# Optimization experiments

Measured on AMD Instinct MI355X. Metric: run time of the kernel, lower is better.

Reference implementation:

```python
import jax, jax.numpy as jnp
import numpy as np

EMBED_DIM = 1024
BATCH, SEQ = 4, 2048


def setup_inputs() -> dict:
    key = jax.random.key(0)
    k1, k2 = jax.random.split(key)
    hidden_states = jax.random.normal(k1, (BATCH, SEQ, EMBED_DIM), dtype=jnp.float32)
    # fused QKV projection weight (Linear(embed_dim, 3*embed_dim, bias=False)),
    # stored as [E, 3E] so y = x @ W
    W_qkv = jax.random.normal(k2, (EMBED_DIM, 3 * EMBED_DIM), dtype=jnp.float32) * (1.0 / np.sqrt(EMBED_DIM))
    return {"hidden_states": hidden_states, "W_qkv": W_qkv}


def reference(hidden_states, W_qkv):
    E = hidden_states.shape[-1]
    scale = 1.0 / np.sqrt(E)
    qkv = jnp.einsum('bse,ef->bsf', hidden_states, W_qkv)  # [B,S,3E]
    q, k, v = jnp.split(qkv, 3, axis=-1)                   # each [B,S,E]
    # scores = q @ (k^T * scale); softmax over keys
    scores = jnp.einsum('bqe,bke->bqk', q, k) * scale      # [B,S,S]
    w = jax.nn.softmax(scores, axis=-1)
    return jnp.einsum('bqk,bke->bqe', w, v)                # [B,S,E]
```

## Files before the change

kernel.cpp:

```cpp
#include <hip/hip_runtime.h>

typedef __attribute__((ext_vector_type(8))) short short8;
typedef __attribute__((ext_vector_type(8))) unsigned short ushort8;
typedef __attribute__((ext_vector_type(4))) float f32x4;

__device__ __forceinline__ float bf2f(unsigned short u) {
  union { unsigned int u; float f; } c; c.u = ((unsigned int)u) << 16; return c.f;
}
__device__ __forceinline__ unsigned short f2bf(float f) {
  union { float f; unsigned int u; } c; c.f = f;
  unsigned int x = c.u;
  return (unsigned short)((x + 0x7FFFu + ((x >> 16) & 1u)) >> 16);
}

#define GLD_LDS16(g, l)                                                        \
  __builtin_amdgcn_global_load_lds(                                            \
      (const __attribute__((address_space(1))) void*)(g),                      \
      (__attribute__((address_space(3))) void*)(l), 16, 0, 0)

__device__ __forceinline__ void bar() {
  asm volatile("" ::: "memory");
  __builtin_amdgcn_s_barrier();
  asm volatile("" ::: "memory");
}

__global__ __launch_bounds__(256) void prep_kernel(
    const float* __restrict__ X, unsigned short* __restrict__ Xb,
    const float* __restrict__ W, unsigned short* __restrict__ Wt,
    float* __restrict__ Lrow) {
  const int t = threadIdx.x;
  if (blockIdx.x < 4096) {
    long i = ((long)blockIdx.x * 256 + t) * 8;
    float4 a = *(const float4*)(X + i);
    float4 b = *(const float4*)(X + i + 4);
    ushort8 o;
    o[0] = f2bf(a.x); o[1] = f2bf(a.y); o[2] = f2bf(a.z); o[3] = f2bf(a.w);
    o[4] = f2bf(b.x); o[5] = f2bf(b.y); o[6] = f2bf(b.z); o[7] = f2bf(b.w);
    *(ushort8*)(Xb + i) = o;
  } else if (blockIdx.x < 4864) {
    const int bid = blockIdx.x - 4096;
    const int f0 = (bid % 48) * 64;
    const int e0 = (bid / 48) * 64;
    __shared__ unsigned short tile[64][65];
    const int cg = (t & 15) * 4;
    const int r = t >> 4;
#pragma unroll
    for (int i = 0; i < 4; ++i) {
      int e = r + i * 16;
      float4 v = *(const float4*)(W + (long)(e0 + e) * 3072 + f0 + cg);
      tile[e][cg + 0] = f2bf(v.x);
      tile[e][cg + 1] = f2bf(v.y);
      tile[e][cg + 2] = f2bf(v.z);
      tile[e][cg + 3] = f2bf(v.w);
    }
    __syncthreads();
#pragma unroll
    for (int i = 0; i < 4; ++i) {
      int f = (t >> 4) + i * 16;
      int e = (t & 15) * 4;
      ushort4 o;
      o.x = tile[e + 0][f];
      o.y = tile[e + 1][f];
      o.z = tile[e + 2][f];
      o.w = tile[e + 3][f];
      *(ushort4*)(Wt + (long)(f0 + f) * 1024 + e0 + e) = o;
    }
  } else {
    float4 z = {0.f, 0.f, 0.f, 0.f};
#pragma unroll
    for (int j = 0; j < 8; ++j) *(float4*)(Lrow + (j * 256 + t) * 4) = z;
  }
}

template <int MODE>
__device__ __forceinline__ void gemm256_body(
    const unsigned short* __restrict__ A, const unsigned short* __restrict__ B,
    void* __restrict__ Cv, int K, int lda, int ldb, int ldc,
    long sA, long sB, long sC, float alpha, float* __restrict__ Lrow,
    unsigned short* __restrict__ Vt) {
  __shared__ __align__(16) unsigned short smem[65536];

  const int t = threadIdx.x;
  const int lane = t & 63;
  const int wave = t >> 6;
  const int quad = lane >> 4;
  const int mrow = lane & 15;
  const int wm = wave >> 2;
  const int wn = wave & 3;

  const int bx = blockIdx.x, by = blockIdx.y, b = blockIdx.z;
  const int rowA0 = by * 256;
  const int rowB0 = bx * 256;
  const unsigned short* Ab = A + (long)b * sA;
  const unsigned short* Bb = B + (long)b * sB;

  const int srow = lane >> 2;
  const int schunk = (lane & 3) * 8;

  f32x4 acc[8][4];
#pragma unroll
  for (int i = 0; i < 8; ++i)
#pragma unroll
    for (int j = 0; j < 4; ++j) {
      f32x4 z = {0.f, 0.f, 0.f, 0.f};
      acc[i][j] = z;
    }

  const int NT = K >> 6;

  auto stg = [&](const unsigned short* gb, int ld, int r0, int kt, int kh,
                 int roff) {
#pragma unroll
    for (int j = 0; j < 2; ++j)
      GLD_LDS16(gb + (long)(r0 + j * 128 + wave * 16 + srow) * ld + kt +
                    kh * 32 + schunk,
                smem + roff + (j * 128 + wave * 16) * 32);
  };

  stg(Ab, lda, rowA0, 0, 0, 0);
  stg(Bb, ldb, rowB0, 0, 0, 16384);
  stg(Ab, lda, rowA0, 0, 1, 8192);
  stg(Bb, ldb, rowB0, 0, 1, 24576);
  stg(Bb, ldb, rowB0, 64, 0, 32768 + 16384);
  stg(Ab, lda, rowA0, 64, 0, 32768);
  asm volatile("s_waitcnt vmcnt(4)" ::: "memory");
  bar();

  const int rA_base = wm * 128 + mrow;
  const int rB_base = wn * 64 + mrow;
  const int qoff = quad * 8;

  for (int T = 0; T < NT; ++T) {
    const int buf = (T & 1) << 15;
    const int nbuf = buf ^ 32768;
    const unsigned short* A0 = smem + buf;
    const unsigned short* A1 = smem + buf + 8192;
    const unsigned short* B0 = smem + buf + 16384;
    const unsigned short* B1 = smem + buf + 24576;
    const int ktn = (T + 1) << 6;
    const int ktn2 = (T + 2) << 6;
    short8 af[4], bf[4];

#pragma unroll
    for (int i = 0; i < 4; ++i)
      af[i] = *(const short8*)(A0 + (rA_base + i * 16) * 32 + qoff);
#pragma unroll
    for (int j = 0; j < 4; ++j)
      bf[j] = *(const short8*)(B0 + (rB_base + j * 16) * 32 + qoff);
    if (T + 1 < NT) stg(Ab, lda, rowA0, ktn, 1, nbuf + 8192);
    bar();
    __builtin_amdgcn_sched_barrier(0);
    __builtin_amdgcn_s_setprio(1);
#pragma unroll
    for (int i = 0; i < 4; ++i)
#pragma unroll
      for (int j = 0; j < 4; ++j)
        acc[i][j] = __builtin_amdgcn_mfma_f32_16x16x32_bf16(af[i], bf[j],
                                                            acc[i][j], 0, 0, 0);
    __builtin_amdgcn_s_setprio(0);
    __builtin_amdgcn_sched_barrier(0);
    bar();

#pragma unroll
    for (int i = 0; i < 4; ++i)
      af[i] = *(const short8*)(A0 + (rA_base + 64 + i * 16) * 32 + qoff);
    if (T + 1 < NT) stg(Bb, ldb, rowB0, ktn, 1, nbuf + 24576);
    bar();
    __builtin_amdgcn_sched_barrier(0);
    __builtin_amdgcn_s_setprio(1);
#pragma unroll
    for (int i = 0; i < 4; ++i)
#pragma unroll
      for (int j = 0; j < 4; ++j)
        acc[4 + i][j] = __builtin_amdgcn_mfma_f32_16x16x32_bf16(
            af[i], bf[j], acc[4 + i][j], 0, 0, 0);
    __builtin_amdgcn_s_setprio(0);
    __builtin_amdgcn_sched_barrier(0);
    bar();

#pragma unroll
    for (int i = 0; i < 4; ++i)
      af[i] = *(const short8*)(A1 + (rA_base + i * 16) * 32 + qoff);
#pragma unroll
    for (int j = 0; j < 4; ++j)
      bf[j] = *(const short8*)(B1 + (rB_base + j * 16) * 32 + qoff);
    if (T + 2 < NT) stg(Bb, ldb, rowB0, ktn2, 0, buf + 16384);
    bar();
    __builtin_amdgcn_sched_barrier(0);
    __builtin_amdgcn_s_setprio(1);
#pragma unroll
    for (int i = 0; i < 4; ++i)
#pragma unroll
      for (int j = 0; j < 4; ++j)
        acc[i][j] = __builtin_amdgcn_mfma_f32_16x16x32_bf16(af[i], bf[j],
                                                            acc[i][j], 0, 0, 0);
    __builtin_amdgcn_s_setprio(0);
    __builtin_amdgcn_sched_barrier(0);
    bar();

#pragma unroll
    for (int i = 0; i < 4; ++i)
      af[i] = *(const short8*)(A1 + (rA_base + 64 + i * 16) * 32 + qoff);
    if (T + 2 < NT) stg(Ab, lda, rowA0, ktn2, 0, buf);
    bar();
    __builtin_amdgcn_sched_barrier(0);
    __builtin_amdgcn_s_setprio(1);
#pragma unroll
    for (int i = 0; i < 4; ++i)
#pragma unroll
      for (int j = 0; j < 4; ++j)
        acc[4 + i][j] = __builtin_amdgcn_mfma_f32_16x16x32_bf16(
            af[i], bf[j], acc[4 + i][j], 0, 0, 0);
    __builtin_amdgcn_s_setprio(0);
    __builtin_amdgcn_sched_barrier(0);
    if (T + 2 < NT) {
      asm volatile("s_waitcnt vmcnt(4)" ::: "memory");
    } else if (T + 1 < NT) {
      asm volatile("s_waitcnt vmcnt(0)" ::: "memory");
    }
    bar();
  }

  const long cb = (long)b * sC;

  if constexpr (MODE == 0) {
    if (bx < 8) {
      unsigned short* C = (unsigned short*)Cv;
#pragma unroll
      for (int m = 0; m < 8; ++m) {
        int row = rowA0 + wm * 128 + m * 16 + quad * 4;
#pragma unroll
        for (int j = 0; j < 4; ++j) {
          int col = rowB0 + wn * 64 + j * 16 + mrow;
#pragma unroll
          for (int r = 0; r < 4; ++r)
            C[(long)(row + r) * ldc + col] = f2bf(acc[m][j][r]);
        }
      }
    } else {
#pragma unroll
      for (int m = 0; m < 8; ++m) {
        int s4 = wm * 128 + m * 16 + quad * 4;
#pragma unroll
        for (int j = 0; j < 4; ++j) {
          int e = wn * 64 + j * 16 + mrow;
          int swz = ((e & 7) << 4) ^ (((e >> 3) & 3) << 3);
          ushort4 pk;
          pk.x = f2bf(acc[m][j][0]);
          pk.y = f2bf(acc[m][j][1]);
          pk.z = f2bf(acc[m][j][2]);
          pk.w = f2bf(acc[m][j][3]);
          *(ushort4*)(smem + e * 256 + (s4 ^ swz)) = pk;
        }
      }
      __syncthreads();
      const int batch = by >> 3;
      const int s_base = (by & 7) * 256;
      const int e_base = (bx - 8) * 256;
      unsigned short* VtB = Vt + (long)batch * 1024 * 2048;
      const int er = t >> 5;
      const int s = (t & 31) * 8;
#pragma unroll
      for (int rnd = 0; rnd < 16; ++rnd) {
        int e = rnd * 16 + er;
        int swz = ((e & 7) << 4) ^ (((e >> 3) & 3) << 3);
        ushort8 v = *(const ushort8*)(smem + e * 256 + (s ^ swz));
        *(ushort8*)(VtB + (long)(e_base + e) * 2048 + s_base + s) = v;
      }
    }
  } else {
    unsigned short* C = (unsigned short*)Cv;
    float p[8][4];
#pragma unroll
    for (int m = 0; m < 8; ++m)
#pragma unroll
      for (int r = 0; r < 4; ++r) p[m][r] = 0.f;
#pragma unroll
    for (int m = 0; m < 8; ++m) {
      int row = rowA0 + wm * 128 + m * 16 + quad * 4;
#pragma unroll
      for (int j = 0; j < 4; ++j) {
        int col = rowB0 + wn * 64 + j * 16 + mrow;
#pragma unroll
        for (int r = 0; r < 4; ++r) {
          float e = __expf(acc[m][j][r] * alpha);
          C[cb + (long)(row + r) * ldc + col] = f2bf(e);
          p[m][r] += e;
        }
      }
    }
#pragma unroll
    for (int off = 1; off < 16; off <<= 1)
#pragma unroll
      for (int m = 0; m < 8; ++m)
#pragma unroll
        for (int r = 0; r < 4; ++r)
          p[m][r] += __shfl_xor(p[m][r], off, 64);
    if (mrow == 0) {
#pragma unroll
      for (int m = 0; m < 8; ++m) {
        int row = rowA0 + wm * 128 + m * 16 + quad * 4;
#pragma unroll
        for (int r = 0; r < 4; ++r)
          atomicAdd(&Lrow[b * 2048 + row + r], p[m][r]);
      }
    }
  }
}

template <int MODE>
__device__ __forceinline__ void gemm_body(
    const unsigned short* __restrict__ A, const unsigned short* __restrict__ B,
    void* __restrict__ Cv, int K, int lda, int ldb, int ldc,
    long sA, long sB, long sC, float alpha, float* __restrict__ Lrow,
    unsigned short* __restrict__ Vt) {
  constexpr int BM = 128, BN = 128, BK = 64;
  __shared__ __align__(16) unsigned short smem[BM * BK + BN * BK];
  unsigned short* As = smem;
  unsigned short* Bs = smem + BM * BK;

  const int t = threadIdx.x;
  const int lane = t & 63;
  const int wave = t >> 6;
  const int quad = lane >> 4;
  const int mrow = lane & 15;
  const int wm = wave >> 1, wn = wave & 1;

  const int bx = blockIdx.x, by = blockIdx.y;
  const int rowA0 = by * BM;
  const int rowB0 = bx * BN;
  const int b = blockIdx.z;
  const unsigned short* Ab = A + (long)b * sA;
  const unsigned short* Bb = B + (long)b * sB;

  f32x4 acc[4][4];
#pragma unroll
  for (int i = 0; i < 4; ++i)
#pragma unroll
    for (int j = 0; j < 4; ++j) {
      f32x4 z = {0.f, 0.f, 0.f, 0.f};
      acc[i][j] = z;
    }

  const int rbase = wave * 32 + (lane >> 3);
  const int c2 = lane & 7;

  for (int kt = 0; kt < K; kt += BK) {
#pragma unroll
    for (int j = 0; j < 4; ++j) {
      int r = rbase + j * 8;
      int c = c2 ^ (r & 7);
      GLD_LDS16(Ab + (long)(rowA0 + r) * lda + kt + c * 8, As + (wave * 4 + j) * 512);
      GLD_LDS16(Bb + (long)(rowB0 + r) * ldb + kt + c * 8, Bs + (wave * 4 + j) * 512);
    }
    __syncthreads();
#pragma unroll
    for (int ks = 0; ks < 2; ++ks) {
      short8 af[4], bfr[4];
#pragma unroll
      for (int i = 0; i < 4; ++i) {
        int rA = wm * 64 + i * 16 + mrow;
        int cc = ks * 4 + quad;
        af[i] = *(const short8*)(As + (rA * 8 + (cc ^ (rA & 7))) * 8);
        int rB = wn * 64 + i * 16 + mrow;
        bfr[i] = *(const short8*)(Bs + (rB * 8 + (cc ^ (rB & 7))) * 8);
      }
#pragma unroll
      for (int mt = 0; mt < 4; ++mt)
#pragma unroll
        for (int nt = 0; nt < 4; ++nt)
          acc[mt][nt] = __builtin_amdgcn_mfma_f32_16x16x32_bf16(
              af[mt], bfr[nt], acc[mt][nt], 0, 0, 0);
    }
    __syncthreads();
  }

  const int m_base = rowA0 + wm * 64;
  const int n_base = rowB0 + wn * 64;
  const long cb = (long)b * sC;

#pragma unroll
  for (int mt = 0; mt < 4; ++mt)
#pragma unroll
    for (int i = 0; i < 4; ++i) {
      int row = m_base + mt * 16 + quad * 4 + i;
      float inv = 1.0f / Lrow[b * 2048 + row];
#pragma unroll
      for (int nt = 0; nt < 4; ++nt) {
        int col = n_base + nt * 16 + mrow;
        ((float*)Cv)[cb + (long)row * ldc + col] = acc[mt][nt][i] * inv;
      }
    }
}

__global__ __launch_bounds__(512, 2) void qkv_gemm_kernel(
    const unsigned short* __restrict__ A, const unsigned short* __restrict__ B,
    void* __restrict__ Cv, int K, int lda, int ldb, int ldc,
    long sA, long sB, long sC, float alpha, float* __restrict__ Lrow,
    unsigned short* __restrict__ Vt) {
  gemm256_body<0>(A, B, Cv, K, lda, ldb, ldc, sA, sB, sC, alpha, Lrow, Vt);
}
__global__ __launch_bounds__(512, 2) void score_gemm_kernel(
    const unsigned short* __restrict__ A, const unsigned short* __restrict__ B,
    void* __restrict__ Cv, int K, int lda, int ldb, int ldc,
    long sA, long sB, long sC, float alpha, float* __restrict__ Lrow,
    unsigned short* __restrict__ Vt) {
  gemm256_body<1>(A, B, Cv, K, lda, ldb, ldc, sA, sB, sC, alpha, Lrow, Vt);
}
__global__ __launch_bounds__(256, 2) void out_gemm_kernel(
    const unsigned short* __restrict__ A, const unsigned short* __restrict__ B,
    void* __restrict__ Cv, int K, int lda, int ldb, int ldc,
    long sA, long sB, long sC, float alpha, float* __restrict__ Lrow,
    unsigned short* __restrict__ Vt) {
  gemm_body<2>(A, B, Cv, K, lda, ldb, ldc, sA, sB, sC, alpha, Lrow, Vt);
}

extern "C" void kernel_launch(void* const* d_in, const int* in_sizes, int n_in,
                              void* d_out, int out_size, void* d_ws, size_t ws_size,
                              hipStream_t stream) {
  const float* X = (const float*)d_in[0];
  const float* W = (const float*)d_in[1];
  float* out = (float*)d_out;

  char* ws = (char*)d_ws;
  unsigned short* Xb  = (unsigned short*)(ws);
  unsigned short* Wtb = (unsigned short*)(ws + 16777216);
  unsigned short* QK  = (unsigned short*)(ws + 23068672);
  unsigned short* Vt  = (unsigned short*)(ws + 56623104);
  unsigned short* Sb  = (unsigned short*)(ws + 73400320);
  float* Lrow         = (float*)(ws + 106954752);

  prep_kernel<<<4865, 256, 0, stream>>>(X, Xb, W, Wtb, Lrow);

  qkv_gemm_kernel<<<dim3(12, 32, 1), 512, 0, stream>>>(
      Xb, Wtb, QK, 1024, 1024, 1024, 2048, 0L, 0L, 0L, 1.0f, nullptr, Vt);

  score_gemm_kernel<<<dim3(8, 8, 4), 512, 0, stream>>>(
      QK, QK + 1024, Sb, 1024, 2048, 2048, 2048,
      (long)2048 * 2048, (long)2048 * 2048, (long)2048 * 2048, 0.03125f, Lrow, nullptr);

  out_gemm_kernel<<<dim3(8, 16, 4), 256, 0, stream>>>(
      Sb, Vt, out, 2048, 2048, 2048, 1024,
      (long)2048 * 2048, (long)1024 * 2048, (long)2048 * 1024, 1.0f, Lrow, nullptr);
}
```

Measured before the change: 250.1 us.

## Use XOR-swizzled 64-wide LDS tiles and restructure the async staging schedule

```diff
diff --git a/kernel.cpp b/kernel.cpp
--- a/kernel.cpp
+++ b/kernel.cpp
@@ -94,8 +94,8 @@
   const unsigned short* Ab = A + (long)b * sA;
   const unsigned short* Bb = B + (long)b * sB;
 
-  const int srow = lane >> 2;
-  const int schunk = (lane & 3) * 8;
+  const int srow = lane >> 3;
+  const int scol = ((lane & 7) ^ srow) * 8;
 
   f32x4 acc[8][4];
 #pragma unroll
@@ -108,46 +108,50 @@
 
   const int NT = K >> 6;
 
-  auto stg = [&](const unsigned short* gb, int ld, int r0, int kt, int kh,
-                 int roff) {
-#pragma unroll
-    for (int j = 0; j < 2; ++j)
-      GLD_LDS16(gb + (long)(r0 + j * 128 + wave * 16 + srow) * ld + kt +
-                    kh * 32 + schunk,
-                smem + roff + (j * 128 + wave * 16) * 32);
+  auto stg = [&](const unsigned short* gb, int ld, int r0, int kt, int j,
+                 int boff) {
+    int rl = j * 64 + wave * 8;
+    GLD_LDS16(gb + (long)(r0 + rl + srow) * ld + kt + scol,
+              smem + boff + rl * 64);
   };
 
-  stg(Ab, lda, rowA0, 0, 0, 0);
-  stg(Bb, ldb, rowB0, 0, 0, 16384);
-  stg(Ab, lda, rowA0, 0, 1, 8192);
-  stg(Bb, ldb, rowB0, 0, 1, 24576);
-  stg(Bb, ldb, rowB0, 64, 0, 32768 + 16384);
-  stg(Ab, lda, rowA0, 64, 0, 32768);
-  asm volatile("s_waitcnt vmcnt(4)" ::: "memory");
-  bar();
-
-  const int rA_base = wm * 128 + mrow;
-  const int rB_base = wn * 64 + mrow;
-  const int qoff = quad * 8;
+  {
+#pragma unroll
+    for (int j = 0; j < 4; ++j) stg(Ab, lda, rowA0, 0, j, 0);
+#pragma unroll
+    for (int j = 0; j < 4; ++j) stg(Bb, ldb, rowB0, 0, j, 16384);
+    if (NT > 1) {
+      stg(Bb, ldb, rowB0, 64, 0, 32768 + 16384);
+      stg(Bb, ldb, rowB0, 64, 1, 32768 + 16384);
+      asm volatile("s_waitcnt vmcnt(2)" ::: "memory");
+    } else {
+      asm volatile("s_waitcnt vmcnt(0)" ::: "memory");
+    }
+    bar();
+  }
+
+  const int m7 = mrow & 7;
+  const int aslot0 = (quad ^ m7) * 8;
 
   for (int T = 0; T < NT; ++T) {
-    const int buf = (T & 1) << 15;
-    const int nbuf = buf ^ 32768;
-    const unsigned short* A0 = smem + buf;
-    const unsigned short* A1 = smem + buf + 8192;
-    const unsigned short* B0 = smem + buf + 16384;
-    const unsigned short* B1 = smem + buf + 24576;
-    const int ktn = (T + 1) << 6;
-    const int ktn2 = (T + 2) << 6;
+    const int boff = (T & 1) << 15;
+    const int noff = boff ^ 32768;
+    const unsigned short* As = smem + boff;
+    const unsigned short* Bs = smem + boff + 16384;
+    const int kt1 = (T + 1) << 6;
+    const int kt2 = (T + 2) << 6;
     short8 af[4], bf[4];
 
 #pragma unroll
     for (int i = 0; i < 4; ++i)
-      af[i] = *(const short8*)(A0 + (rA_base + i * 16) * 32 + qoff);
+      af[i] = *(const short8*)(As + (wm * 128 + i * 16 + mrow) * 64 + aslot0);
 #pragma unroll
     for (int j = 0; j < 4; ++j)
-      bf[j] = *(const short8*)(B0 + (rB_base + j * 16) * 32 + qoff);
-    if (T + 1 < NT) stg(Ab, lda, rowA0, ktn, 1, nbuf + 8192);
+      bf[j] = *(const short8*)(Bs + (wn * 64 + j * 16 + mrow) * 64 + aslot0);
+    if (T + 1 < NT) {
+      stg(Ab, lda, rowA0, kt1, 0, noff);
+      stg(Ab, lda, rowA0, kt1, 2, noff);
+    }
     bar();
     __builtin_amdgcn_sched_barrier(0);
     __builtin_amdgcn_s_setprio(1);
@@ -163,8 +167,12 @@
 
 #pragma unroll
     for (int i = 0; i < 4; ++i)
-      af[i] = *(const short8*)(A0 + (rA_base + 64 + i * 16) * 32 + qoff);
-    if (T + 1 < NT) stg(Bb, ldb, rowB0, ktn, 1, nbuf + 24576);
+      af[i] =
+          *(const short8*)(As + (wm * 128 + 64 + i * 16 + mrow) * 64 + aslot0);
+    if (T + 1 < NT) {
+      stg(Ab, lda, rowA0, kt1, 1, noff);
+      stg(Ab, lda, rowA0, kt1, 3, noff);
+    }
     bar();
     __builtin_amdgcn_sched_barrier(0);
     __builtin_amdgcn_s_setprio(1);
@@ -180,11 +188,16 @@
 
 #pragma unroll
     for (int i = 0; i < 4; ++i)
-      af[i] = *(const short8*)(A1 + (rA_base + i * 16) * 32 + qoff);
+      af[i] = *(const short8*)(As + (wm * 128 + i * 16 + mrow) * 64 +
+                               (aslot0 ^ 32));
 #pragma unroll
     for (int j = 0; j < 4; ++j)
-      bf[j] = *(const short8*)(B1 + (rB_base + j * 16) * 32 + qoff);
-    if (T + 2 < NT) stg(Bb, ldb, rowB0, ktn2, 0, buf + 16384);
+      bf[j] = *(const short8*)(Bs + (wn * 64 + j * 16 + mrow) * 64 +
+                               (aslot0 ^ 32));
+    if (T + 1 < NT) {
+      stg(Bb, ldb, rowB0, kt1, 2, noff + 16384);
+      stg(Bb, ldb, rowB0, kt1, 3, noff + 16384);
+    }
     bar();
     __builtin_amdgcn_sched_barrier(0);
     __builtin_amdgcn_s_setprio(1);
@@ -200,8 +213,12 @@
 
 #pragma unroll
     for (int i = 0; i < 4; ++i)
-      af[i] = *(const short8*)(A1 + (rA_base + 64 + i * 16) * 32 + qoff);
-    if (T + 2 < NT) stg(Ab, lda, rowA0, ktn2, 0, buf);
+      af[i] = *(const short8*)(As + (wm * 128 + 64 + i * 16 + mrow) * 64 +
+                               (aslot0 ^ 32));
+    if (T + 2 < NT) {
+      stg(Bb, ldb, rowB0, kt2, 0, boff + 16384);
+      stg(Bb, ldb, rowB0, kt2, 1, boff + 16384);
+    }
     bar();
     __builtin_amdgcn_sched_barrier(0);
     __builtin_amdgcn_s_setprio(1);
@@ -214,8 +231,8 @@
     __builtin_amdgcn_s_setprio(0);
     __builtin_amdgcn_sched_barrier(0);
     if (T + 2 < NT) {
-      asm volatile("s_waitcnt vmcnt(4)" ::: "memory");
-    } else if (T + 1 < NT) {
+      asm volatile("s_waitcnt vmcnt(2)" ::: "memory");
+    } else {
       asm volatile("s_waitcnt vmcnt(0)" ::: "memory");
     }
     bar();
```

After: 239.1 us. -4.4%, faster.
